# Performance work log

Hardware: AMD Instinct MI355X
Metric: run time of the kernel (lower is better)

## Reference

```python
import jax, jax.numpy as jnp
import numpy as np

DT = 0.01
NLAG = 50           # int(maxlag / dt), maxlag = 0.5 s
NMA = 20
NC = 8192
NT = 4096


def _xcorr(data1, data2):
    # torch F.conv1d(data1.view(1, nc, nt), data2.view(nc, 1, nt),
    #                padding=NLAG+1, groups=nc)
    # == per-channel sliding cross-correlation.
    lhs = data1[None]            # (1, NC, NT)
    rhs = data2[:, None, :]      # (NC, 1, NT) -- one tiny filter per group
    out = jax.lax.conv_general_dilated(
        lhs, rhs,
        window_strides=(1,),
        padding=[(NLAG + 1, NLAG + 1)],
        dimension_numbers=("NCH", "OIH", "NCH"),
        feature_group_count=NC,
    )
    return out                   # (1, NC, L), L = 2*NLAG + 3 when nt1 == nt2


def _moving_average(x, nma=NMA):
    # Faithful to CCModel.moving_average: AvgPool1d(nma, stride=1, pad=nma//2)
    # applied after permute(0,2,1), i.e. the pooling runs over the CHANNEL
    # axis, with zero padding included in the mean (count_include_pad=True),
    # then sliced back to nc channels.
    nb, nc, L = x.shape
    pad = nma // 2
    xp = jnp.pad(x, ((0, 0), (pad, pad), (0, 0)))
    cs = jnp.concatenate(
        [jnp.zeros((nb, 1, L), x.dtype), jnp.cumsum(xp, axis=1)], axis=1)
    win = (cs[:, nma:, :] - cs[:, :-nma, :]) / nma   # sliding sum / nma
    return win[:, :nc, :]


def _pick_maxabs(R, dt):
    # pick_Rkt_maxabs: per-channel max-|cc| pick.
    L = R.shape[-1]
    nlag_c = (L - 1) // 2        # zero-lag index
    imax = jnp.argmax(jnp.abs(R), axis=-1)                              # (nb, nc)
    vmain = jnp.take_along_axis(R, imax[..., None], axis=-1)[..., 0]    # signed peak
    vpos = jnp.max(R, axis=-1)
    vneg = jnp.min(R, axis=-1)
    vside = jnp.where(vmain >= 0, vneg, vpos)        # opposite-sign extremum
    tmax = (imax - nlag_c).astype(R.dtype) * dt
    return vmain, vside, tmax


def setup_inputs() -> dict:
    key = jax.random.key(0)
    k1, k2, k3, k4 = jax.random.split(key, 4)
    data1 = jax.random.normal(k1, (NC, NT), dtype=jnp.float32)
    data2 = jax.random.normal(k2, (NC, NT), dtype=jnp.float32)
    event1 = jax.random.randint(k3, (1,), 0, 1000, dtype=jnp.int32)
    event2 = jax.random.randint(k4, (1,), 0, 1000, dtype=jnp.int32)
    return {"data1": data1, "data2": data2, "event1": event1, "event2": event2}


def reference(data1, data2, event1, event2):
    xcor = _xcorr(data1, data2)              # (1, NC, 2*NLAG+3)
    xcor = _moving_average(xcor, NMA)        # in-place overwrite in torch
    vmax, vmin, tmax = _pick_maxabs(xcor, DT)
    return xcor, vmax, vmin, tmax
```

## Files before the change

kernel.cpp:

```cpp
#include <hip/hip_runtime.h>

#define NC 8192
#define NT 4096
#define NLAGS 103
#define WS_STRIDE 104
#define XBASE (NC*NLAGS)

#define D1LOG 4208
#define D1DW  4224
#define D2DW  4096
#define REDS  29
#define SMEMF (D1DW + D2DW)

__device__ __forceinline__ int swz(int b) {
    return b ^ (((b >> 7) & 7) << 4);
}

__global__ __launch_bounds__(256, 4)
void xcorr_kernel(const float* __restrict__ g1, const float* __restrict__ g2,
                  float* __restrict__ ws) {
    __shared__ __align__(128) float smem[SMEMF];
    char* d1b = (char*)smem;
    char* d2b = (char*)(smem + D1DW);
    const int tid  = threadIdx.x;
    const int wv   = tid >> 6;
    const int lane = tid & 63;
    const int c    = blockIdx.x;
    const float* g1c = g1 + (size_t)c * NT;
    const float* g2c = g2 + (size_t)c * NT;

    #pragma unroll
    for (int t = 0; t < 4; ++t) {
        const int O = 4096*wv + 1024*t + 16*lane;
        const int S = O ^ ((lane >> 3) << 4);
        __builtin_amdgcn_global_load_lds(
            (const float*)((const char*)g2c + S),
            (float*)(d2b + 4096*wv + 1024*t),
            16, 0, 0);
    }

    {
        const float4* r = (const float4*)g1c;
        float4 v0 = r[tid], v1 = r[tid+256], v2 = r[tid+512], v3 = r[tid+768];
        if (tid < 52) *(float*)(d1b + swz(4*tid)) = 0.f;
        if (tid < 60) *(float*)(d1b + swz(4*(4148 + tid))) = 0.f;
        const int B = 208 + 16*tid;
        *(float4*)(d1b + swz(B))         = v0;
        *(float4*)(d1b + swz(B + 4096))  = v1;
        *(float4*)(d1b + swz(B + 8192))  = v2;
        *(float4*)(d1b + swz(B + 12288)) = v3;
    }
    __syncthreads();

    float acc[28];
    #pragma unroll
    for (int l = 0; l < 28; ++l) acc[l] = 0.f;

    #pragma unroll 1
    for (int it = 0; it < 2; ++it) {
        const int k0 = 2048*it + 32*lane;
        float b[32];
        {
            const int base = 128*lane + 8192*it;
            const int sx   = (lane & 7) << 4;
            #pragma unroll
            for (int t = 0; t < 8; ++t) {
                float4 v = *(const float4*)(d2b + ((base + 16*t) ^ sx));
                b[4*t]=v.x; b[4*t+1]=v.y; b[4*t+2]=v.z; b[4*t+3]=v.w;
            }
        }
        float w[60];
        {
            const int xb = 4*(k0 + 28*wv);
            #pragma unroll
            for (int t = 0; t < 15; ++t) {
                float4 v = *(const float4*)(d1b + swz(xb + 16*t));
                w[4*t]=v.x; w[4*t+1]=v.y; w[4*t+2]=v.z; w[4*t+3]=v.w;
            }
        }
        #pragma unroll
        for (int j = 0; j < 32; ++j)
            #pragma unroll
            for (int l = 0; l < 28; ++l)
                acc[l] = fmaf(w[l+j], b[j], acc[l]);
    }

    __syncthreads();
    #pragma unroll
    for (int l = 0; l < 28; ++l) acc[l] += __shfl_down(acc[l], 32);
    float* red = (float*)d2b + wv * (32*REDS);
    if (lane < 32) {
        #pragma unroll
        for (int l = 0; l < 28; ++l) red[lane*REDS + l] = acc[l];
    }
    if (lane < 28) {
        float s = 0.f;
        #pragma unroll
        for (int r = 0; r < 32; ++r) s += red[r*REDS + lane];
        const int L = 28*wv + lane - 1;
        if (L >= 0 && L < NLAGS) ws[(size_t)c * WS_STRIDE + L] = s;
    }
}

#define TS 112
__global__ __launch_bounds__(256, 4)
void ma_pick_kernel(const float* __restrict__ ws, float* __restrict__ out) {
    __shared__ float tile[52*TS];
    __shared__ float matile[32*TS];
    const int tid = threadIdx.x;
    const int c0  = blockIdx.x * 32;

    for (int i = tid; i < 52*TS; i += 256) {
        int r   = i / TS;
        int col = i - r*TS;
        int g   = c0 - 10 + r;
        float v = 0.f;
        if (g >= 0 && g < NC && col < NLAGS) v = ws[(size_t)g*WS_STRIDE + col];
        tile[i] = v;
    }
    __syncthreads();

    {
        const int l = tid & 127;
        const int h = tid >> 7;
        if (l < NLAGS) {
            const int cc0 = h * 16;
            float s = 0.f;
            #pragma unroll
            for (int r = 0; r < 20; ++r) s += tile[(cc0 + r)*TS + l];
            #pragma unroll 1
            for (int cc = cc0; cc < cc0 + 16; ++cc) {
                float ma = s / 20.0f;
                matile[cc*TS + l] = ma;
                out[(size_t)(c0 + cc)*NLAGS + l] = ma;
                s += tile[(cc + 20)*TS + l] - tile[cc*TS + l];
            }
        }
    }
    __syncthreads();

    const int wv = tid >> 6, lane = tid & 63;
    #pragma unroll 1
    for (int s8 = 0; s8 < 8; ++s8) {
        const int cc = wv*8 + s8;
        float v1 = matile[cc*TS + lane];
        float a1 = fabsf(v1);
        int   i1 = lane;
        float vmx = v1, vmn = v1;
        if (lane < NLAGS - 64) {
            float v2 = matile[cc*TS + 64 + lane];
            float a2 = fabsf(v2);
            vmx = fmaxf(vmx, v2); vmn = fminf(vmn, v2);
            if (a2 > a1) { a1 = a2; i1 = 64 + lane; v1 = v2; }
        }
        #pragma unroll
        for (int d = 32; d >= 1; d >>= 1) {
            float oa  = __shfl_xor(a1, d);
            int   oi  = __shfl_xor(i1, d);
            float ov  = __shfl_xor(v1, d);
            float omx = __shfl_xor(vmx, d);
            float omn = __shfl_xor(vmn, d);
            vmx = fmaxf(vmx, omx);
            vmn = fminf(vmn, omn);
            if (oa > a1 || (oa == a1 && oi < i1)) { a1 = oa; i1 = oi; v1 = ov; }
        }
        if (lane == 0) {
            const int ch = c0 + cc;
            out[XBASE + ch]        = v1;
            out[XBASE + NC + ch]   = (v1 >= 0.f) ? vmn : vmx;
            out[XBASE + 2*NC + ch] = (float)(i1 - 51) * 0.01f;
        }
    }
}

extern "C" void kernel_launch(void* const* d_in, const int* in_sizes, int n_in,
                              void* d_out, int out_size, void* d_ws, size_t ws_size,
                              hipStream_t stream) {
    const float* g1 = (const float*)d_in[0];
    const float* g2 = (const float*)d_in[1];
    float* out = (float*)d_out;
    float* ws  = (float*)d_ws;

    hipLaunchKernelGGL(xcorr_kernel, dim3(NC), dim3(256), 0, stream, g1, g2, ws);
    hipLaunchKernelGGL(ma_pick_kernel, dim3(NC/32), dim3(256), 0, stream, ws, out);
}
```

Baseline: 314.7 us.

## Replace XOR swizzle with granule permutation layout and split inner loop into halves

Replaces the XOR-based LDS swizzle with a 16-byte-granule permutation (Pg/Pinv) for both data1 and data2 shared buffers, folding zero-padding into the load loop. The inner correlation loop is split into two halves of 16 taps each with a scheduling barrier, shrinking the live register window (b and w arrays) to reduce register pressure and LDS bank conflicts. This trades extra address arithmetic and an extra LDS load pass for lower VGPR use and potentially better occupancy.

```diff
diff --git a/kernel.cpp b/kernel.cpp
--- a/kernel.cpp
+++ b/kernel.cpp
@@ -6,22 +6,24 @@
 #define WS_STRIDE 104
 #define XBASE (NC*NLAGS)
 
-#define D1LOG 4208
-#define D1DW  4224
-#define D2DW  4096
-#define REDS  29
-#define SMEMF (D1DW + D2DW)
+__device__ __forceinline__ int Pg(int q) {
+    return (q & ~127) | ((q & 7) << 4) | ((q >> 3) & 15);
+}
+__device__ __forceinline__ int Pinv(int p) {
+    return (p & ~127) | ((p & 15) << 3) | ((p >> 4) & 7);
+}
 
-__device__ __forceinline__ int swz(int b) {
-    return b ^ (((b >> 7) & 7) << 4);
-}
+#define D1GR 1152
+#define D2GR 1024
+#define SMEMDW ((D1GR + D2GR)*4)
+#define REDS 29
 
 __global__ __launch_bounds__(256, 4)
 void xcorr_kernel(const float* __restrict__ g1, const float* __restrict__ g2,
                   float* __restrict__ ws) {
-    __shared__ __align__(128) float smem[SMEMF];
+    __shared__ __align__(128) float smem[SMEMDW];
     char* d1b = (char*)smem;
-    char* d2b = (char*)(smem + D1DW);
+    char* d2b = (char*)smem + D1GR*16;
     const int tid  = threadIdx.x;
     const int wv   = tid >> 6;
     const int lane = tid & 63;
@@ -31,24 +33,24 @@
 
     #pragma unroll
     for (int t = 0; t < 4; ++t) {
-        const int O = 4096*wv + 1024*t + 16*lane;
-        const int S = O ^ ((lane >> 3) << 4);
+        const int j = 4*wv + t;
+        const int q = Pinv(64*j + lane);
         __builtin_amdgcn_global_load_lds(
-            (const float*)((const char*)g2c + S),
-            (float*)(d2b + 4096*wv + 1024*t),
+            (const float*)((const char*)g2c + 16*q),
+            (float*)(d2b + 1024*j),
             16, 0, 0);
     }
 
-    {
-        const float4* r = (const float4*)g1c;
-        float4 v0 = r[tid], v1 = r[tid+256], v2 = r[tid+512], v3 = r[tid+768];
-        if (tid < 52) *(float*)(d1b + swz(4*tid)) = 0.f;
-        if (tid < 60) *(float*)(d1b + swz(4*(4148 + tid))) = 0.f;
-        const int B = 208 + 16*tid;
-        *(float4*)(d1b + swz(B))         = v0;
-        *(float4*)(d1b + swz(B + 4096))  = v1;
-        *(float4*)(d1b + swz(B + 8192))  = v2;
-        *(float4*)(d1b + swz(B + 12288)) = v3;
+    #pragma unroll
+    for (int t = 0; t < 5; ++t) {
+        const int p = tid + 256*t;
+        if (p < D1GR) {
+            const int q = Pinv(p);
+            float4 v = make_float4(0.f, 0.f, 0.f, 0.f);
+            if (q >= 13 && q < 1037)
+                v = *(const float4*)((const char*)g1c + 16*q - 208);
+            *(float4*)(d1b + 16*p) = v;
+        }
     }
     __syncthreads();
 
@@ -58,31 +60,29 @@
 
     #pragma unroll 1
     for (int it = 0; it < 2; ++it) {
-        const int k0 = 2048*it + 32*lane;
-        float b[32];
-        {
-            const int base = 128*lane + 8192*it;
-            const int sx   = (lane & 7) << 4;
+        const int qb = 512*it + 8*lane;
+        const int qa = qb + 7*wv;
+        #pragma unroll
+        for (int h = 0; h < 2; ++h) {
+            float b[16];
             #pragma unroll
-            for (int t = 0; t < 8; ++t) {
-                float4 v = *(const float4*)(d2b + ((base + 16*t) ^ sx));
+            for (int t = 0; t < 4; ++t) {
+                float4 v = *(const float4*)(d2b + 16*Pg(qb + 4*h + t));
                 b[4*t]=v.x; b[4*t+1]=v.y; b[4*t+2]=v.z; b[4*t+3]=v.w;
             }
-        }
-        float w[60];
-        {
-            const int xb = 4*(k0 + 28*wv);
+            float w[44];
             #pragma unroll
-            for (int t = 0; t < 15; ++t) {
-                float4 v = *(const float4*)(d1b + swz(xb + 16*t));
+            for (int t = 0; t < 11; ++t) {
+                float4 v = *(const float4*)(d1b + 16*Pg(qa + 4*h + t));
                 w[4*t]=v.x; w[4*t+1]=v.y; w[4*t+2]=v.z; w[4*t+3]=v.w;
             }
+            #pragma unroll
+            for (int j = 0; j < 16; ++j)
+                #pragma unroll
+                for (int l = 0; l < 28; ++l)
+                    acc[l] = fmaf(w[l+j], b[j], acc[l]);
+            __builtin_amdgcn_sched_barrier(0);
         }
-        #pragma unroll
-        for (int j = 0; j < 32; ++j)
-            #pragma unroll
-            for (int l = 0; l < 28; ++l)
-                acc[l] = fmaf(w[l+j], b[j], acc[l]);
     }
 
     __syncthreads();
```

After: 316.5 us. About the same (+0.6%).
